# Optimization experiments

Measured on AMD Instinct MI355X. Metric: run time of the kernel, lower is better.

## Reference

```python
import jax, jax.numpy as jnp
import numpy as np

CLAMP = 60.0
EPS = 1e-4

def _make_weights(N, alpha_logits, delta_logits, beta_logits):
    alpha = jax.nn.sigmoid(alpha_logits)   # [C,H]
    delta = jax.nn.sigmoid(delta_logits)
    beta = jax.nn.sigmoid(beta_logits)
    A = alpha * beta                        # [C,H]
    r = jnp.clip(1.0 - alpha * delta, EPS, 1.0 - EPS)
    t = jnp.arange(N, dtype=jnp.float32)[:, None, None]   # [N,1,1]
    logr = jnp.clip(jnp.log(r) * t, -CLAMP, CLAMP)        # [N,C,H]
    return A, jnp.exp(logr), jnp.exp(-logr)

def _ema_fwd(x, A, eta, r_pos, r_neg):
    # x: [B,N,C] -> y: [B,N,C]
    z = A * x[..., None] * r_neg            # [B,N,C,H]
    h = jnp.cumsum(z, axis=1) * r_pos       # [B,N,C,H]
    return jnp.sum(eta * h, axis=-1)        # [B,N,C]

def reference(x, alpha_logits, delta_logits, beta_logits, eta, proj_w, proj_b):
    B, N, C = x.shape
    A, r_pos, r_neg = _make_weights(N, alpha_logits, delta_logits, beta_logits)
    xf = x.astype(jnp.float32)
    y_fwd = _ema_fwd(xf, A, eta, r_pos, r_neg)
    y_bwd = _ema_fwd(xf[:, ::-1], A, eta, r_pos, r_neg)[:, ::-1]
    z = jnp.concatenate([y_fwd, y_bwd], axis=-1).astype(x.dtype)  # [B,N,2C]
    return z @ proj_w.T + proj_b            # [B,N,C]

def setup_inputs():
    key = jax.random.key(0)
    ks = jax.random.split(key, 7)
    B, N, C, H = 8, 4096, 512, 4
    return {
        "x": jax.random.normal(ks[0], (B, N, C), dtype=jnp.float32),
        "alpha_logits": jax.random.normal(ks[1], (C, H), dtype=jnp.float32),
        "delta_logits": jax.random.normal(ks[2], (C, H), dtype=jnp.float32),
        "beta_logits": jax.random.normal(ks[3], (C, H), dtype=jnp.float32),
        "eta": jax.random.normal(ks[4], (C, H), dtype=jnp.float32) * 0.02,
        "proj_w": jax.random.normal(ks[5], (C, 2 * C), dtype=jnp.float32) / np.sqrt(2.0 * C),
        "proj_b": jax.random.normal(ks[6], (C,), dtype=jnp.float32) * 0.01,
    }
```

## Files before the change

kernel.cpp:

```cpp
#include <hip/hip_runtime.h>
#include <hip/hip_bf16.h>

#define B_ 8
#define N_ 4096
#define C_ 512
#define H_ 4
#define EPS_ 1e-4f
#define E60P 1.14200739e26f
#define E60M 8.7565108e-27f

typedef __attribute__((ext_vector_type(8))) short short8;
typedef __attribute__((ext_vector_type(4))) float floatx4;
typedef __attribute__((ext_vector_type(2))) float floatx2;
typedef __attribute__((ext_vector_type(4))) unsigned short ushort4_t;
typedef unsigned short ushort_t;

__device__ __forceinline__ float sigmoidf_(float v) {
    return 1.0f / (1.0f + expf(-v));
}

__device__ __forceinline__ int pk_off(int t, int w, int k0, int ks, int f,
                                      int lane8, int kb) {
    return ((((t * 2 + w) * 16 + k0) * 2 + ks) * 4 + f) * 512 + lane8 * 8 + kb;
}

__device__ __forceinline__ void gload16(const void* g, void* l) {
    __builtin_amdgcn_global_load_lds(
        (const __attribute__((address_space(1))) void*)g,
        (__attribute__((address_space(3))) void*)l, 16, 0, 0);
}

__global__ __launch_bounds__(256, 8) void k_partials5(
    const float* __restrict__ x, const float* __restrict__ al,
    const float* __restrict__ dl, const float* __restrict__ bl,
    float* __restrict__ P)
{
    int bid   = blockIdx.x;
    int chunk = bid & 15;
    int ct    = (bid >> 4) & 7;
    int b     = (bid >> 7) & 7;
    int dir   = bid >> 10;
    int lane  = threadIdx.x & 63;
    int wave  = threadIdx.x >> 6;
    int c     = ct * 64 + lane;
    int sub   = chunk * 4 + wave;
    int t0f   = sub * 64;
    int t0b   = (63 - sub) * 64;

    float aa[4], dd[4], bb[4];
    { float4 v = ((const float4*)al)[c]; aa[0]=v.x; aa[1]=v.y; aa[2]=v.z; aa[3]=v.w; }
    { float4 v = ((const float4*)dl)[c]; dd[0]=v.x; dd[1]=v.y; dd[2]=v.z; dd[3]=v.w; }
    { float4 v = ((const float4*)bl)[c]; bb[0]=v.x; bb[1]=v.y; bb[2]=v.z; bb[3]=v.w; }

    float A[H_], ri[H_], Lh[H_];
    #pragma unroll
    for (int h = 0; h < H_; ++h) {
        float alpha = sigmoidf_(aa[h]);
        float delta = sigmoidf_(dd[h]);
        float beta  = sigmoidf_(bb[h]);
        A[h] = alpha * beta;
        float r = fminf(fmaxf(1.0f - alpha * delta, EPS_), 1.0f - EPS_);
        Lh[h] = logf(r);
        ri[h] = 1.0f / r;
    }
    floatx2 ri2[2]  = {{ri[0], ri[1]}, {ri[2], ri[3]}};
    floatx2 AEP2[2] = {{A[0] * E60P, A[1] * E60P}, {A[2] * E60P, A[3] * E60P}};

    const float* xp = x + ((size_t)b * N_ + t0f) * C_ + c;

    int   t0   = dir ? t0b : t0f;
    floatx2 Ae2[2], T2[2];
    #pragma unroll
    for (int p = 0; p < 2; ++p) {
        Ae2[p] = (floatx2){A[2*p]   * expf(fminf(-Lh[2*p]   * (float)t0, 60.0f)),
                           A[2*p+1] * expf(fminf(-Lh[2*p+1] * (float)t0, 60.0f))};
        T2[p]  = (floatx2){0.f, 0.f};
    }

    if (dir == 0) {
        float cur[8];
        #pragma unroll
        for (int j = 0; j < 8; ++j) cur[j] = xp[(size_t)j * C_];
        #pragma unroll 1
        for (int g = 0; g < 8; ++g) {
            float nxt[8];
            if (g < 7) {
                #pragma unroll
                for (int j = 0; j < 8; ++j)
                    nxt[j] = xp[(size_t)(g * 8 + 8 + j) * C_];
            }
            #pragma unroll
            for (int j = 0; j < 8; ++j) {
                floatx2 xv2 = {cur[j], cur[j]};
                #pragma unroll
                for (int p = 0; p < 2; ++p) {
                    T2[p] += Ae2[p] * xv2;
                    Ae2[p] = __builtin_elementwise_min(Ae2[p] * ri2[p], AEP2[p]);
                }
            }
            if (g < 7) {
                #pragma unroll
                for (int j = 0; j < 8; ++j) cur[j] = nxt[j];
            }
        }
        float* pp = P + ((size_t)b * 64 + sub) * (H_ * C_) + c;
        pp[0]      = T2[0].x;  pp[C_]     = T2[0].y;
        pp[2 * C_] = T2[1].x;  pp[3 * C_] = T2[1].y;
    } else {
        float cur[8];
        #pragma unroll
        for (int j = 0; j < 8; ++j) cur[j] = xp[(size_t)(63 - j) * C_];
        #pragma unroll 1
        for (int g = 0; g < 8; ++g) {
            float nxt[8];
            if (g < 7) {
                #pragma unroll
                for (int j = 0; j < 8; ++j)
                    nxt[j] = xp[(size_t)(63 - (g * 8 + 8 + j)) * C_];
            }
            #pragma unroll
            for (int j = 0; j < 8; ++j) {
                floatx2 xv2 = {cur[j], cur[j]};
                #pragma unroll
                for (int p = 0; p < 2; ++p) {
                    T2[p] += Ae2[p] * xv2;
                    Ae2[p] = __builtin_elementwise_min(Ae2[p] * ri2[p], AEP2[p]);
                }
            }
            if (g < 7) {
                #pragma unroll
                for (int j = 0; j < 8; ++j) cur[j] = nxt[j];
            }
        }
        float* pp = P + ((size_t)(8 + b) * 64 + (63 - sub)) * (H_ * C_) + c;
        pp[0]      = T2[0].x;  pp[C_]     = T2[0].y;
        pp[2 * C_] = T2[1].x;  pp[3 * C_] = T2[1].y;
    }
}

__global__ __launch_bounds__(256) void k_scan(float* __restrict__ P)
{
    int bid = blockIdx.x;
    int ct  = bid & 7;
    int b   = (bid >> 3) & 7;
    int dir = bid >> 6;
    int cl  = threadIdx.x & 63;
    int h   = threadIdx.x >> 6;
    int c   = ct * 64 + cl;

    float* base = P + ((size_t)(dir * 8 + b) * 64) * (H_ * C_) + h * C_ + c;

    float v[64];
    #pragma unroll
    for (int s = 0; s < 64; ++s) v[s] = base[s * (H_ * C_)];

    float run = 0.0f;
    #pragma unroll
    for (int s = 0; s < 64; ++s) { float t = v[s]; v[s] = run; run += t; }

    #pragma unroll
    for (int s = 0; s < 64; ++s) base[s * (H_ * C_)] = v[s];
}

__global__ __launch_bounds__(256, 5) void k_apply6(
    const float* __restrict__ x, const float* __restrict__ al,
    const float* __restrict__ dl, const float* __restrict__ bl,
    const float* __restrict__ eta, const float* __restrict__ P,
    ushort_t* __restrict__ Zp)
{
    __shared__ __align__(16) ushort_t zlds[4][4096];

    int bid   = blockIdx.x;
    int chunk = bid & 15;
    int ct    = (bid >> 4) & 7;
    int b     = (bid >> 7) & 7;
    int dir   = bid >> 10;
    int lane  = threadIdx.x & 63;
    int wave  = threadIdx.x >> 6;
    int c     = ct * 64 + lane;
    int sub   = chunk * 4 + wave;
    int t0f   = sub * 64;
    int t0b   = (63 - sub) * 64;

    int mt  = b * 32 + (t0f >> 7);
    int wq  = (t0f >> 6) & 1;
    char* zw = (char*)&zlds[wave][0];

    float aa[4], dd[4], bb[4], ee[4];
    { float4 v = ((const float4*)al )[c]; aa[0]=v.x; aa[1]=v.y; aa[2]=v.z; aa[3]=v.w; }
    { float4 v = ((const float4*)dl )[c]; dd[0]=v.x; dd[1]=v.y; dd[2]=v.z; dd[3]=v.w; }
    { float4 v = ((const float4*)bl )[c]; bb[0]=v.x; bb[1]=v.y; bb[2]=v.z; bb[3]=v.w; }
    { float4 v = ((const float4*)eta)[c]; ee[0]=v.x; ee[1]=v.y; ee[2]=v.z; ee[3]=v.w; }

    float A[H_], rr[H_], ri[H_], Lh[H_];
    #pragma unroll
    for (int h = 0; h < H_; ++h) {
        float alpha = sigmoidf_(aa[h]);
        float delta = sigmoidf_(dd[h]);
        float beta  = sigmoidf_(bb[h]);
        A[h] = alpha * beta;
        float r = fminf(fmaxf(1.0f - alpha * delta, EPS_), 1.0f - EPS_);
        Lh[h] = logf(r);
        rr[h] = r;
        ri[h] = 1.0f / r;
    }
    const floatx2 E2M = {E60M, E60M};
    floatx2 ri2[2]  = {{ri[0], ri[1]}, {ri[2], ri[3]}};
    floatx2 rr2[2]  = {{rr[0], rr[1]}, {rr[2], rr[3]}};
    floatx2 ee2[2]  = {{ee[0], ee[1]}, {ee[2], ee[3]}};
    floatx2 AEP2[2] = {{A[0] * E60P, A[1] * E60P}, {A[2] * E60P, A[3] * E60P}};

    const float* xp = x + ((size_t)b * N_ + t0f) * C_ + c;

    if (dir == 0) {
        const float* cp = P + ((size_t)b * 64 + sub) * (H_ * C_) + c;
        floatx2 Ae2[2], em2[2], S2[2];
        #pragma unroll
        for (int p = 0; p < 2; ++p) {
            Ae2[p] = (floatx2){A[2*p]   * expf(fminf(-Lh[2*p]   * (float)t0f, 60.0f)),
                               A[2*p+1] * expf(fminf(-Lh[2*p+1] * (float)t0f, 60.0f))};
            em2[p] = (floatx2){expf(fmaxf( Lh[2*p]   * (float)t0f, -60.0f)),
                               expf(fmaxf( Lh[2*p+1] * (float)t0f, -60.0f))};
            S2[p]  = (floatx2){cp[(2*p) * C_], cp[(2*p+1) * C_]};
        }
        float cur[8];
        #pragma unroll
        for (int j = 0; j < 8; ++j) cur[j] = xp[(size_t)j * C_];
        #pragma unroll 1
        for (int g = 0; g < 8; ++g) {
            float nxt[8];
            if (g < 7) {
                #pragma unroll
                for (int j = 0; j < 8; ++j)
                    nxt[j] = xp[(size_t)(g * 8 + 8 + j) * C_];
            }
            #pragma unroll
            for (int j = 0; j < 8; ++j) {
                int i = g * 8 + j;
                floatx2 xv2 = {cur[j], cur[j]};
                floatx2 acc = {0.f, 0.f};
                #pragma unroll
                for (int p = 0; p < 2; ++p) {
                    S2[p] += Ae2[p] * xv2;
                    Ae2[p] = __builtin_elementwise_min(Ae2[p] * ri2[p], AEP2[p]);
                    acc   += ee2[p] * (em2[p] * S2[p]);
                    em2[p] = __builtin_elementwise_max(em2[p] * rr2[p], E2M);
                }
                float y = acc.x + acc.y;
                __hip_bfloat16 yb = __float2bfloat16(y);
                int bo = (i * 128 + lane * 2) ^ ((i & 7) << 4);
                *(ushort_t*)(zw + bo) = *(ushort_t*)&yb;
            }
            if (g < 7) {
                #pragma unroll
                for (int j = 0; j < 8; ++j) cur[j] = nxt[j];
            }
        }
    } else {
        const float* cp = P + ((size_t)(8 + b) * 64 + (63 - sub)) * (H_ * C_) + c;
        floatx2 Ae2[2], em2[2], S2[2];
        #pragma unroll
        for (int p = 0; p < 2; ++p) {
            Ae2[p] = (floatx2){A[2*p]   * expf(fminf(-Lh[2*p]   * (float)t0b, 60.0f)),
                               A[2*p+1] * expf(fminf(-Lh[2*p+1] * (float)t0b, 60.0f))};
            em2[p] = (floatx2){expf(fmaxf( Lh[2*p]   * (float)t0b, -60.0f)),
                               expf(fmaxf( Lh[2*p+1] * (float)t0b, -60.0f))};
            S2[p]  = (floatx2){cp[(2*p) * C_], cp[(2*p+1) * C_]};
        }
        float cur[8];
        #pragma unroll
        for (int j = 0; j < 8; ++j) cur[j] = xp[(size_t)(63 - j) * C_];
        #pragma unroll 1
        for (int g = 0; g < 8; ++g) {
            float nxt[8];
            if (g < 7) {
                #pragma unroll
                for (int j = 0; j < 8; ++j)
                    nxt[j] = xp[(size_t)(63 - (g * 8 + 8 + j)) * C_];
            }
            #pragma unroll
            for (int j = 0; j < 8; ++j) {
                int i = 63 - (g * 8 + j);
                floatx2 xv2 = {cur[j], cur[j]};
                floatx2 acc = {0.f, 0.f};
                #pragma unroll
                for (int p = 0; p < 2; ++p) {
                    S2[p] += Ae2[p] * xv2;
                    Ae2[p] = __builtin_elementwise_min(Ae2[p] * ri2[p], AEP2[p]);
                    acc   += ee2[p] * (em2[p] * S2[p]);
                    em2[p] = __builtin_elementwise_max(em2[p] * rr2[p], E2M);
                }
                float y = acc.x + acc.y;
                __hip_bfloat16 yb = __float2bfloat16(y);
                int bo = (i * 128 + lane * 2) ^ ((i & 7) << 4);
                *(ushort_t*)(zw + bo) = *(ushort_t*)&yb;
            }
            if (g < 7) {
                #pragma unroll
                for (int j = 0; j < 8; ++j) cur[j] = nxt[j];
            }
        }
    }

    __syncthreads();

    {
        int k0c = dir ? (8 + ct) : ct;
        size_t cb = ((size_t)((mt * 2 + wq) * 16 + k0c)) * 4096;
        #pragma unroll
        for (int ks = 0; ks < 2; ++ks)
            #pragma unroll
            for (int f = 0; f < 4; ++f) {
                int row = f * 16 + (lane & 15);
                int rb  = (row * 128 + ks * 64 + (lane >> 4) * 16) ^ ((row & 7) << 4);
                short8 v = *(const short8*)(zw + rb);
                *(short8*)(Zp + cb + (ks * 4 + f) * 512 + lane * 8) = v;
            }
    }
}

__global__ __launch_bounds__(256) void k_cvtw2(const float* __restrict__ w,
                                               ushort_t* __restrict__ Wp)
{
    int i4 = blockIdx.x * 256 + threadIdx.x;
    int i  = i4 << 2;
    int n = i >> 10, k = i & 1023;
    int nt = n >> 7, rn = n & 127;
    int k0 = k >> 6, kk = k & 63;
    int off = pk_off(nt, rn >> 6, k0, kk >> 5, (rn >> 4) & 3,
                     ((kk >> 3) & 3) * 16 + (rn & 15), kk & 7);
    float4 v = ((const float4*)w)[i4];
    ushort4_t r;
    { __hip_bfloat16 t = __float2bfloat16(v.x); r.x = *(ushort_t*)&t; }
    { __hip_bfloat16 t = __float2bfloat16(v.y); r.y = *(ushort_t*)&t; }
    { __hip_bfloat16 t = __float2bfloat16(v.z); r.z = *(ushort_t*)&t; }
    { __hip_bfloat16 t = __float2bfloat16(v.w); r.w = *(ushort_t*)&t; }
    *(ushort4_t*)&Wp[off] = r;
}

__global__ __launch_bounds__(256, 4) void k_gemm3(
    const ushort_t* __restrict__ Zp, const ushort_t* __restrict__ Wp,
    const float* __restrict__ bias, float* __restrict__ out)
{
    __shared__ __align__(16) char lds[32768];
    char*  ldsA = lds;
    char*  ldsB = lds + 16384;
    float* stg  = (float*)lds;

    int tid  = threadIdx.x;
    int lane = tid & 63, wave = tid >> 6;
    int wm   = wave & 1, wn = wave >> 1;
    int fr   = lane & 15, quad = lane >> 4;

    int bid = blockIdx.x;
    int mt  = ((bid >> 5) << 3) | (bid & 7);
    int nt  = (bid >> 3) & 3;
    int m0  = mt * 128, n0 = nt * 128;

    const ushort_t* Az = Zp + ((size_t)(mt * 2) * 16) * 4096;
    const ushort_t* Bz = Wp + ((size_t)(nt * 2) * 16) * 4096;

    floatx4 acc[4][4];
    #pragma unroll
    for (int mf = 0; mf < 4; ++mf)
        #pragma unroll
        for (int nf = 0; nf < 4; ++nf)
            acc[mf][nf] = (floatx4){0.f, 0.f, 0.f, 0.f};

    for (int k0 = 0; k0 < 16; ++k0) {
        const ushort_t* As = Az + (size_t)k0 * 4096;
        const ushort_t* Bs = Bz + (size_t)k0 * 4096;
        #pragma unroll
        for (int w = 0; w < 2; ++w)
            #pragma unroll
            for (int inst = 0; inst < 2; ++inst) {
                gload16(As + w * 65536 + inst * 2048 + tid * 8,
                        ldsA + w * 8192 + inst * 4096 + tid * 16);
                gload16(Bs + w * 65536 + inst * 2048 + tid * 8,
                        ldsB + w * 8192 + inst * 4096 + tid * 16);
            }
        asm volatile("s_waitcnt vmcnt(0)" ::: "memory");
        __syncthreads();

        #pragma unroll
        for (int ks = 0; ks < 2; ++ks) {
            short8 af[4], bf[4];
            #pragma unroll
            for (int f = 0; f < 4; ++f) {
                af[f] = *(const short8*)(ldsA + wm * 8192 + (ks * 4 + f) * 1024 + lane * 16);
                bf[f] = *(const short8*)(ldsB + wn * 8192 + (ks * 4 + f) * 1024 + lane * 16);
            }
            #pragma unroll
            for (int mf = 0; mf < 4; ++mf)
                #pragma unroll
                for (int nf = 0; nf < 4; ++nf)
                    acc[mf][nf] = __builtin_amdgcn_mfma_f32_16x16x32_bf16(
                        af[mf], bf[nf], acc[mf][nf], 0, 0, 0);
        }
        __syncthreads();
    }

    int rrow = tid >> 3;
    int seg  = tid & 7;
    int gcol = n0 + seg * 16;

    #pragma unroll
    for (int ch = 0; ch < 4; ++ch) {
        if ((wave & 1) == (ch >> 1)) {
            int ml = (ch & 1) * 2;
            #pragma unroll
            for (int mi = 0; mi < 2; ++mi) {
                #pragma unroll
                for (int nf = 0; nf < 4; ++nf) {
                    int col = wn * 64 + nf * 16 + fr;
                    #pragma unroll
                    for (int rg = 0; rg < 4; ++rg) {
                        int row = mi * 16 + quad * 4 + rg;
                        stg[row * 132 + col] = acc[ml + mi][nf][rg];
                    }
                }
            }
        }
        __syncthreads();
        {
            int gm = m0 + ch * 32 + rrow;
            const float* s = &stg[rrow * 132 + seg * 16];
            #pragma unroll
            for (int k = 0; k < 4; ++k) {
                float4 v  = *(const float4*)&s[k * 4];
                float4 bv = *(const float4*)&bias[gcol + k * 4];
                v.x += bv.x; v.y += bv.y; v.z += bv.z; v.w += bv.w;
                *(float4*)&out[(size_t)gm * 512 + gcol + k * 4] = v;
            }
        }
        __syncthreads();
    }
}

extern "C" void kernel_launch(void* const* d_in, const int* in_sizes, int n_in,
                              void* d_out, int out_size, void* d_ws, size_t ws_size,
                              hipStream_t stream)
{
    const float* x  = (const float*)d_in[0];
    const float* al = (const float*)d_in[1];
    const float* dl = (const float*)d_in[2];
    const float* bl = (const float*)d_in[3];
    const float* et = (const float*)d_in[4];
    const float* pw = (const float*)d_in[5];
    const float* pb = (const float*)d_in[6];
    float* out = (float*)d_out;

    ushort_t* Zp = (ushort_t*)d_ws;
    float*    P  = (float*)((char*)d_ws + 67108864);
    ushort_t* Wp = (ushort_t*)((char*)d_ws + 75497472);

    hipLaunchKernelGGL(k_cvtw2,     dim3(512),  dim3(256), 0, stream, pw, Wp);
    hipLaunchKernelGGL(k_partials5, dim3(2048), dim3(256), 0, stream, x, al, dl, bl, P);
    hipLaunchKernelGGL(k_scan,      dim3(128),  dim3(256), 0, stream, P);
    hipLaunchKernelGGL(k_apply6,    dim3(2048), dim3(256), 0, stream, x, al, dl, bl, et, P, Zp);
    hipLaunchKernelGGL(k_gemm3,     dim3(1024), dim3(256), 0, stream, Zp, Wp, pb, out);
}
```

Measured before the change: 220.5 us.

## Double-buffer GEMM LDS tiles and fold weight conversion into partials kernel

The GEMM now keeps two LDS buffers of 32KB each, so it issues the global-to-LDS loads for tile k+1 before running the MFMAs on tile k. This replaces the old load, wait, compute sequence with overlapped loads and compute, at the cost of doubled LDS and a lower occupancy bound. Separately, the bf16 weight pack kernel is folded into the partials kernel as 512 extra blocks, which removes one kernel launch and lets the conversion run alongside the scan partials.

Result: no change. 221.3 us (+0.4%).

```diff
diff --git a/kernel.cpp b/kernel.cpp
--- a/kernel.cpp
+++ b/kernel.cpp
@@ -30,11 +30,166 @@
         (__attribute__((address_space(3))) void*)l, 16, 0, 0);
 }
 
-__global__ __launch_bounds__(256, 8) void k_partials5(
+__global__ __launch_bounds__(256, 8) void k_partials6(
     const float* __restrict__ x, const float* __restrict__ al,
     const float* __restrict__ dl, const float* __restrict__ bl,
-    float* __restrict__ P)
+    float* __restrict__ P,
+    const float* __restrict__ pw, ushort_t* __restrict__ Wp)
 {
+    int bid   = blockIdx.x;
+
+    if (bid >= 2048) {
+        int i4 = (bid - 2048) * 256 + threadIdx.x;
+        int i  = i4 << 2;
+        int n = i >> 10, k = i & 1023;
+        int nt = n >> 7, rn = n & 127;
+        int k0 = k >> 6, kk = k & 63;
+        int off = pk_off(nt, rn >> 6, k0, kk >> 5, (rn >> 4) & 3,
+                         ((kk >> 3) & 3) * 16 + (rn & 15), kk & 7);
+        float4 v = ((const float4*)pw)[i4];
+        ushort4_t r;
+        { __hip_bfloat16 t = __float2bfloat16(v.x); r.x = *(ushort_t*)&t; }
+        { __hip_bfloat16 t = __float2bfloat16(v.y); r.y = *(ushort_t*)&t; }
+        { __hip_bfloat16 t = __float2bfloat16(v.z); r.z = *(ushort_t*)&t; }
+        { __hip_bfloat16 t = __float2bfloat16(v.w); r.w = *(ushort_t*)&t; }
+        *(ushort4_t*)&Wp[off] = r;
+        return;
+    }
+
+    int chunk = bid & 15;
+    int ct    = (bid >> 4) & 7;
+    int b     = (bid >> 7) & 7;
+    int dir   = bid >> 10;
+    int lane  = threadIdx.x & 63;
+    int wave  = threadIdx.x >> 6;
+    int c     = ct * 64 + lane;
+    int sub   = chunk * 4 + wave;
+    int t0f   = sub * 64;
+    int t0b   = (63 - sub) * 64;
+
+    float aa[4], dd[4], bb[4];
+    { float4 v = ((const float4*)al)[c]; aa[0]=v.x; aa[1]=v.y; aa[2]=v.z; aa[3]=v.w; }
+    { float4 v = ((const float4*)dl)[c]; dd[0]=v.x; dd[1]=v.y; dd[2]=v.z; dd[3]=v.w; }
+    { float4 v = ((const float4*)bl)[c]; bb[0]=v.x; bb[1]=v.y; bb[2]=v.z; bb[3]=v.w; }
+
+    float A[H_], ri[H_], Lh[H_];
+    #pragma unroll
+    for (int h = 0; h < H_; ++h) {
+        float alpha = sigmoidf_(aa[h]);
+        float delta = sigmoidf_(dd[h]);
+        float beta  = sigmoidf_(bb[h]);
+        A[h] = alpha * beta;
+        float r = fminf(fmaxf(1.0f - alpha * delta, EPS_), 1.0f - EPS_);
+        Lh[h] = logf(r);
+        ri[h] = 1.0f / r;
+    }
+    floatx2 ri2[2]  = {{ri[0], ri[1]}, {ri[2], ri[3]}};
+    floatx2 AEP2[2] = {{A[0] * E60P, A[1] * E60P}, {A[2] * E60P, A[3] * E60P}};
+
+    const float* xp = x + ((size_t)b * N_ + t0f) * C_ + c;
+
+    int   t0   = dir ? t0b : t0f;
+    floatx2 Ae2[2], T2[2];
+    #pragma unroll
+    for (int p = 0; p < 2; ++p) {
+        Ae2[p] = (floatx2){A[2*p]   * expf(fminf(-Lh[2*p]   * (float)t0, 60.0f)),
+                           A[2*p+1] * expf(fminf(-Lh[2*p+1] * (float)t0, 60.0f))};
+        T2[p]  = (floatx2){0.f, 0.f};
+    }
+
+    if (dir == 0) {
+        float cur[8];
+        #pragma unroll
+        for (int j = 0; j < 8; ++j) cur[j] = xp[(size_t)j * C_];
+        #pragma unroll 1
+        for (int g = 0; g < 8; ++g) {
+            float nxt[8];
+            if (g < 7) {
+                #pragma unroll
+                for (int j = 0; j < 8; ++j)
+                    nxt[j] = xp[(size_t)(g * 8 + 8 + j) * C_];
+            }
+            #pragma unroll
+            for (int j = 0; j < 8; ++j) {
+                floatx2 xv2 = {cur[j], cur[j]};
+                #pragma unroll
+                for (int p = 0; p < 2; ++p) {
+                    T2[p] += Ae2[p] * xv2;
+                    Ae2[p] = __builtin_elementwise_min(Ae2[p] * ri2[p], AEP2[p]);
+                }
+            }
+            if (g < 7) {
+                #pragma unroll
+                for (int j = 0; j < 8; ++j) cur[j] = nxt[j];
+            }
+        }
+        float* pp = P + ((size_t)b * 64 + sub) * (H_ * C_) + c;
+        pp[0]      = T2[0].x;  pp[C_]     = T2[0].y;
+        pp[2 * C_] = T2[1].x;  pp[3 * C_] = T2[1].y;
+    } else {
+        float cur[8];
+        #pragma unroll
+        for (int j = 0; j < 8; ++j) cur[j] = xp[(size_t)(63 - j) * C_];
+        #pragma unroll 1
+        for (int g = 0; g < 8; ++g) {
+            float nxt[8];
+            if (g < 7) {
+                #pragma unroll
+                for (int j = 0; j < 8; ++j)
+                    nxt[j] = xp[(size_t)(63 - (g * 8 + 8 + j)) * C_];
+            }
+            #pragma unroll
+            for (int j = 0; j < 8; ++j) {
+                floatx2 xv2 = {cur[j], cur[j]};
+                #pragma unroll
+                for (int p = 0; p < 2; ++p) {
+                    T2[p] += Ae2[p] * xv2;
+                    Ae2[p] = __builtin_elementwise_min(Ae2[p] * ri2[p], AEP2[p]);
+                }
+            }
+            if (g < 7) {
+                #pragma unroll
+                for (int j = 0; j < 8; ++j) cur[j] = nxt[j];
+            }
+        }
+        float* pp = P + ((size_t)(8 + b) * 64 + (63 - sub)) * (H_ * C_) + c;
+        pp[0]      = T2[0].x;  pp[C_]     = T2[0].y;
+        pp[2 * C_] = T2[1].x;  pp[3 * C_] = T2[1].y;
+    }
+}
+
+__global__ __launch_bounds__(256) void k_scan(float* __restrict__ P)
+{
+    int bid = blockIdx.x;
+    int ct  = bid & 7;
+    int b   = (bid >> 3) & 7;
+    int dir = bid >> 6;
+    int cl  = threadIdx.x & 63;
+    int h   = threadIdx.x >> 6;
+    int c   = ct * 64 + cl;
+
+    float* base = P + ((size_t)(dir * 8 + b) * 64) * (H_ * C_) + h * C_ + c;
+
+    float v[64];
+    #pragma unroll
+    for (int s = 0; s < 64; ++s) v[s] = base[s * (H_ * C_)];
+
+    float run = 0.0f;
+    #pragma unroll
+    for (int s = 0; s < 64; ++s) { float t = v[s]; v[s] = run; run += t; }
+
+    #pragma unroll
+    for (int s = 0; s < 64; ++s) base[s * (H_ * C_)] = v[s];
+}
+
+__global__ __launch_bounds__(256, 5) void k_apply6(
+    const float* __restrict__ x, const float* __restrict__ al,
+    const float* __restrict__ dl, const float* __restrict__ bl,
+    const float* __restrict__ eta, const float* __restrict__ P,
+    ushort_t* __restrict__ Zp)
+{
+    __shared__ __align__(16) ushort_t zlds[4][4096];
+
     int bid   = blockIdx.x;
     int chunk = bid & 15;
     int ct    = (bid >> 4) & 7;
@@ -47,141 +202,6 @@
     int t0f   = sub * 64;
     int t0b   = (63 - sub) * 64;
 
-    float aa[4], dd[4], bb[4];
-    { float4 v = ((const float4*)al)[c]; aa[0]=v.x; aa[1]=v.y; aa[2]=v.z; aa[3]=v.w; }
-    { float4 v = ((const float4*)dl)[c]; dd[0]=v.x; dd[1]=v.y; dd[2]=v.z; dd[3]=v.w; }
-    { float4 v = ((const float4*)bl)[c]; bb[0]=v.x; bb[1]=v.y; bb[2]=v.z; bb[3]=v.w; }
-
-    float A[H_], ri[H_], Lh[H_];
-    #pragma unroll
-    for (int h = 0; h < H_; ++h) {
-        float alpha = sigmoidf_(aa[h]);
-        float delta = sigmoidf_(dd[h]);
-        float beta  = sigmoidf_(bb[h]);
-        A[h] = alpha * beta;
-        float r = fminf(fmaxf(1.0f - alpha * delta, EPS_), 1.0f - EPS_);
-        Lh[h] = logf(r);
-        ri[h] = 1.0f / r;
-    }
-    floatx2 ri2[2]  = {{ri[0], ri[1]}, {ri[2], ri[3]}};
-    floatx2 AEP2[2] = {{A[0] * E60P, A[1] * E60P}, {A[2] * E60P, A[3] * E60P}};
-
-    const float* xp = x + ((size_t)b * N_ + t0f) * C_ + c;
-
-    int   t0   = dir ? t0b : t0f;
-    floatx2 Ae2[2], T2[2];
-    #pragma unroll
-    for (int p = 0; p < 2; ++p) {
-        Ae2[p] = (floatx2){A[2*p]   * expf(fminf(-Lh[2*p]   * (float)t0, 60.0f)),
-                           A[2*p+1] * expf(fminf(-Lh[2*p+1] * (float)t0, 60.0f))};
-        T2[p]  = (floatx2){0.f, 0.f};
-    }
-
-    if (dir == 0) {
-        float cur[8];
-        #pragma unroll
-        for (int j = 0; j < 8; ++j) cur[j] = xp[(size_t)j * C_];
-        #pragma unroll 1
-        for (int g = 0; g < 8; ++g) {
-            float nxt[8];
-            if (g < 7) {
-                #pragma unroll
-                for (int j = 0; j < 8; ++j)
-                    nxt[j] = xp[(size_t)(g * 8 + 8 + j) * C_];
-            }
-            #pragma unroll
-            for (int j = 0; j < 8; ++j) {
-                floatx2 xv2 = {cur[j], cur[j]};
-                #pragma unroll
-                for (int p = 0; p < 2; ++p) {
-                    T2[p] += Ae2[p] * xv2;
-                    Ae2[p] = __builtin_elementwise_min(Ae2[p] * ri2[p], AEP2[p]);
-                }
-            }
-            if (g < 7) {
-                #pragma unroll
-                for (int j = 0; j < 8; ++j) cur[j] = nxt[j];
-            }
-        }
-        float* pp = P + ((size_t)b * 64 + sub) * (H_ * C_) + c;
-        pp[0]      = T2[0].x;  pp[C_]     = T2[0].y;
-        pp[2 * C_] = T2[1].x;  pp[3 * C_] = T2[1].y;
-    } else {
-        float cur[8];
-        #pragma unroll
-        for (int j = 0; j < 8; ++j) cur[j] = xp[(size_t)(63 - j) * C_];
-        #pragma unroll 1
-        for (int g = 0; g < 8; ++g) {
-            float nxt[8];
-            if (g < 7) {
-                #pragma unroll
-                for (int j = 0; j < 8; ++j)
-                    nxt[j] = xp[(size_t)(63 - (g * 8 + 8 + j)) * C_];
-            }
-            #pragma unroll
-            for (int j = 0; j < 8; ++j) {
-                floatx2 xv2 = {cur[j], cur[j]};
-                #pragma unroll
-                for (int p = 0; p < 2; ++p) {
-                    T2[p] += Ae2[p] * xv2;
-                    Ae2[p] = __builtin_elementwise_min(Ae2[p] * ri2[p], AEP2[p]);
-                }
-            }
-            if (g < 7) {
-                #pragma unroll
-                for (int j = 0; j < 8; ++j) cur[j] = nxt[j];
-            }
-        }
-        float* pp = P + ((size_t)(8 + b) * 64 + (63 - sub)) * (H_ * C_) + c;
-        pp[0]      = T2[0].x;  pp[C_]     = T2[0].y;
-        pp[2 * C_] = T2[1].x;  pp[3 * C_] = T2[1].y;
-    }
-}
-
-__global__ __launch_bounds__(256) void k_scan(float* __restrict__ P)
-{
-    int bid = blockIdx.x;
-    int ct  = bid & 7;
-    int b   = (bid >> 3) & 7;
-    int dir = bid >> 6;
-    int cl  = threadIdx.x & 63;
-    int h   = threadIdx.x >> 6;
-    int c   = ct * 64 + cl;
-
-    float* base = P + ((size_t)(dir * 8 + b) * 64) * (H_ * C_) + h * C_ + c;
-
-    float v[64];
-    #pragma unroll
-    for (int s = 0; s < 64; ++s) v[s] = base[s * (H_ * C_)];
-
-    float run = 0.0f;
-    #pragma unroll
-    for (int s = 0; s < 64; ++s) { float t = v[s]; v[s] = run; run += t; }
-
-    #pragma unroll
-    for (int s = 0; s < 64; ++s) base[s * (H_ * C_)] = v[s];
-}
-
-__global__ __launch_bounds__(256, 5) void k_apply6(
-    const float* __restrict__ x, const float* __restrict__ al,
-    const float* __restrict__ dl, const float* __restrict__ bl,
-    const float* __restrict__ eta, const float* __restrict__ P,
-    ushort_t* __restrict__ Zp)
-{
-    __shared__ __align__(16) ushort_t zlds[4][4096];
-
-    int bid   = blockIdx.x;
-    int chunk = bid & 15;
-    int ct    = (bid >> 4) & 7;
-    int b     = (bid >> 7) & 7;
-    int dir   = bid >> 10;
-    int lane  = threadIdx.x & 63;
-    int wave  = threadIdx.x >> 6;
-    int c     = ct * 64 + lane;
-    int sub   = chunk * 4 + wave;
-    int t0f   = sub * 64;
-    int t0b   = (63 - sub) * 64;
-
     int mt  = b * 32 + (t0f >> 7);
     int wq  = (t0f >> 6) & 1;
     char* zw = (char*)&zlds[wave][0];
@@ -319,33 +339,12 @@
     }
 }
 
-__global__ __launch_bounds__(256) void k_cvtw2(const float* __restrict__ w,
-                                               ushort_t* __restrict__ Wp)
-{
-    int i4 = blockIdx.x * 256 + threadIdx.x;
-    int i  = i4 << 2;
-    int n = i >> 10, k = i & 1023;
-    int nt = n >> 7, rn = n & 127;
-    int k0 = k >> 6, kk = k & 63;
-    int off = pk_off(nt, rn >> 6, k0, kk >> 5, (rn >> 4) & 3,
-                     ((kk >> 3) & 3) * 16 + (rn & 15), kk & 7);
-    float4 v = ((const float4*)w)[i4];
-    ushort4_t r;
-    { __hip_bfloat16 t = __float2bfloat16(v.x); r.x = *(ushort_t*)&t; }
-    { __hip_bfloat16 t = __float2bfloat16(v.y); r.y = *(ushort_t*)&t; }
-    { __hip_bfloat16 t = __float2bfloat16(v.z); r.z = *(ushort_t*)&t; }
-    { __hip_bfloat16 t = __float2bfloat16(v.w); r.w = *(ushort_t*)&t; }
-    *(ushort4_t*)&Wp[off] = r;
-}
-
-__global__ __launch_bounds__(256, 4) void k_gemm3(
+__global__ __launch_bounds__(256, 2) void k_gemm5(
     const ushort_t* __restrict__ Zp, const ushort_t* __restrict__ Wp,
     const float* __restrict__ bias, float* __restrict__ out)
 {
-    __shared__ __align__(16) char lds[32768];
-    char*  ldsA = lds;
-    char*  ldsB = lds + 16384;
-    float* stg  = (float*)lds;
+    __shared__ __align__(16) char lds[65536];
+    float* stg = (float*)lds;
 
     int tid  = threadIdx.x;
     int lane = tid & 63, wave = tid >> 6;
@@ -367,7 +366,9 @@
         for (int nf = 0; nf < 4; ++nf)
             acc[mf][nf] = (floatx4){0.f, 0.f, 0.f, 0.f};
 
-    for (int k0 = 0; k0 < 16; ++k0) {
+    auto STAGE = [&](int bi, int k0) {
+        char* ldsA = lds + bi * 32768;
+        char* ldsB = ldsA + 16384;
         const ushort_t* As = Az + (size_t)k0 * 4096;
         const ushort_t* Bs = Bz + (size_t)k0 * 4096;
         #pragma unroll
@@ -379,26 +380,42 @@
                 gload16(Bs + w * 65536 + inst * 2048 + tid * 8,
                         ldsB + w * 8192 + inst * 4096 + tid * 16);
             }
-        asm volatile("s_waitcnt vmcnt(0)" ::: "memory");
-        __syncthreads();
-
-        #pragma unroll
-        for (int ks = 0; ks < 2; ++ks) {
-            short8 af[4], bf[4];
+    };
+
+    STAGE(0, 0);
+    asm volatile("s_waitcnt vmcnt(0)" ::: "memory");
+    __syncthreads();
+
+    int cur = 0;
+    for (int k0 = 0; k0 < 16; ++k0) {
+        if (k0 < 15) STAGE(cur ^ 1, k0 + 1);
+        __builtin_amdgcn_sched_barrier(0);
+        char* ldsA = lds + cur * 32768;
+        char* ldsB = ldsA + 16384;
+        short8 af[2][4], bf[2][4];
+        #pragma unroll
+        for (int ks = 0; ks < 2; ++ks)
             #pragma unroll
             for (int f = 0; f < 4; ++f) {
-                af[f] = *(const short8*)(ldsA + wm * 8192 + (ks * 4 + f) * 1024 + lane * 16);
-                bf[f] = *(const short8*)(ldsB + wn * 8192 + (ks * 4 + f) * 1024 + lane * 16);
-            }
+                af[ks][f] = *(const short8*)(ldsA + wm * 8192 + (ks * 4 + f) * 1024 + lane * 16);
+                bf[ks][f] = *(const short8*)(ldsB + wn * 8192 + (ks * 4 + f) * 1024 + lane * 16);
+            }
+        #pragma unroll
+        for (int ks = 0; ks < 2; ++ks)
             #pragma unroll
             for (int mf = 0; mf < 4; ++mf)
                 #pragma unroll
                 for (int nf = 0; nf < 4; ++nf)
                     acc[mf][nf] = __builtin_amdgcn_mfma_f32_16x16x32_bf16(
-                        af[mf], bf[nf], acc[mf][nf], 0, 0, 0);
-        }
-        __syncthreads();
-    }
+                        af[ks][mf], bf[ks][nf], acc[mf][nf], 0, 0, 0);
+        if (k0 < 15) {
+            __builtin_amdgcn_sched_barrier(0);
+            asm volatile("s_waitcnt vmcnt(0)" ::: "memory");
+            __syncthreads();
+            cur ^= 1;
+        }
+    }
+    __syncthreads();
 
     int rrow = tid >> 3;
     int seg  = tid & 7;
@@ -454,9 +471,11 @@
     float*    P  = (float*)((char*)d_ws + 67108864);
     ushort_t* Wp = (ushort_t*)((char*)d_ws + 75497472);
 
-    hipLaunchKernelGGL(k_cvtw2,     dim3(512),  dim3(256), 0, stream, pw, Wp);
-    hipLaunchKernelGGL(k_partials5, dim3(2048), dim3(256), 0, stream, x, al, dl, bl, P);
+    hipLaunchKernelGGL(k_partials6, dim3(2560), dim3(256), 0, stream,
+                       x, al, dl, bl, P, pw, Wp);
     hipLaunchKernelGGL(k_scan,      dim3(128),  dim3(256), 0, stream, P);
-    hipLaunchKernelGGL(k_apply6,    dim3(2048), dim3(256), 0, stream, x, al, dl, bl, et, P, Zp);
-    hipLaunchKernelGGL(k_gemm3,     dim3(1024), dim3(256), 0, stream, Zp, Wp, pb, out);
-}
+    hipLaunchKernelGGL(k_apply6,    dim3(2048), dim3(256), 0, stream,
+                       x, al, dl, bl, et, P, Zp);
+    hipLaunchKernelGGL(k_gemm5,     dim3(1024), dim3(256), 0, stream,
+                       Zp, Wp, pb, out);
+}
```
